# Performance work log

Measured on AMD Instinct MI355X. Metric: run time of the kernel, lower is better.

The kernel has to match this reference:

```python
import jax, jax.numpy as jnp
import numpy as np

NUM_SAMPLES = 32  # S: Gibbs chains per datapoint


def setup_inputs() -> dict:
    key = jax.random.key(0)
    ks = jax.random.split(key, 6)
    N, F, M, C = 2048, 1024, 128, 100
    x = jax.random.normal(ks[0], (N, F), dtype=jnp.float32)
    y = jax.random.randint(ks[1], (N,), 0, C)
    alpha_0 = jax.random.normal(ks[2], (M,), dtype=jnp.float32)
    alpha = jax.random.normal(ks[3], (M, F), dtype=jnp.float32) * jnp.float32(2.0 / np.sqrt(F))
    beta_0 = jax.random.normal(ks[4], (C,), dtype=jnp.float32)
    beta = jax.random.normal(ks[5], (C, M), dtype=jnp.float32) * jnp.float32(2.0 / np.sqrt(M))
    return {"x": x, "y": y, "alpha_0": alpha_0, "alpha": alpha, "beta_0": beta_0, "beta": beta}


def _gibbs_and_loglik(x, y, alpha_0, alpha, beta_0, beta):
    S = NUM_SAMPLES
    N = x.shape[0]
    C, M = beta.shape
    y_onehot = jax.nn.one_hot(y, C, dtype=x.dtype)           # (N, C)

    # compute_linear_pi / compute_pi_pos (pi_pos is no_grad in original)
    linear_pi = alpha_0[None, :] + x @ alpha.T               # (N, M)
    pi_pos = jax.lax.stop_gradient(jax.nn.sigmoid(linear_pi))

    key = jax.random.key(42)
    k_init, k_gibbs = jax.random.split(key)

    # init_sample2: Z ~ 2*Bernoulli(pi_pos) - 1, sampled S times  (no_grad)
    Z0 = 2.0 * jax.random.bernoulli(k_init, pi_pos, (S, N, M)).astype(x.dtype) - 1.0

    beta_sg = jax.lax.stop_gradient(beta)
    beta0_sg = jax.lax.stop_gradient(beta_0)

    # class logits for current Z; maintained incrementally across Gibbs steps
    lin0 = beta0_sg[None, None, :] + jnp.einsum('snm,cm->snc', Z0, beta_sg)  # (S, N, C)

    order = jnp.asarray(np.random.RandomState(0).permutation(M))  # fixed Gibbs sweep order
    keys = jax.random.split(k_gibbs, M)

    def step(carry, inp):
        Z, lin = carry
        j, k = inp
        zj = jnp.take(Z, j, axis=2)           # (S, N) current value of coord j
        bj = jnp.take(beta_sg, j, axis=1)     # (C,)
        pij = jnp.take(pi_pos, j, axis=1)     # (N,)
        # logits if coord j were +1 / -1 (rank-1 update of lin)
        lin_pos = lin + (1.0 - zj)[..., None] * bj
        lin_neg = lin + (-1.0 - zj)[..., None] * bj
        g_pos = jnp.exp(jnp.einsum('nc,snc->sn', y_onehot, lin_pos)) / jnp.sum(jnp.exp(lin_pos), axis=2)
        g_neg = jnp.exp(jnp.einsum('nc,snc->sn', y_onehot, lin_neg)) / jnp.sum(jnp.exp(lin_neg), axis=2)
        num = g_pos * pij[None, :]
        p = num / (num + g_neg * (1.0 - pij)[None, :])
        znew = 2.0 * jax.random.bernoulli(k, p).astype(lin.dtype) - 1.0  # (S, N)
        lin = lin + (znew - zj)[..., None] * bj
        Z = jax.lax.dynamic_update_index_in_dim(Z, znew, j, axis=2)
        return (Z, lin), None

    (Z, _), _ = jax.lax.scan(step, (Z0, lin0), (order, keys))
    Z = jax.lax.stop_gradient(Z)

    # moments
    EI = jnp.mean((Z + 1.0) * 0.5, axis=0)                   # (N, M)
    EII = jnp.mean(Z, axis=0)                                # (N, M)
    linear_gamma = beta_0[None, None, :] + jnp.einsum('snm,cm->snc', Z, beta)
    EIII = jnp.mean(jax.nn.logsumexp(linear_gamma, axis=2), axis=0)  # (N,)

    TermI = jnp.sum(y_onehot * (beta_0[None, :] + EII @ beta.T))
    TermII = jnp.sum(EIII)
    TermIII = jnp.sum(EI * linear_pi)
    TermIV = jnp.sum(jax.nn.softplus(linear_pi))             # log(1 + exp(linear_pi)), stable
    return TermI - TermII + TermIII - TermIV


def reference(x, y, alpha_0, alpha, beta_0, beta):
    return _gibbs_and_loglik(x, y, alpha_0, alpha, beta_0, beta)
```

## Files before the change

kernel.cpp:

```cpp
#include <hip/hip_runtime.h>
#include <hip/hip_fp16.h>
#include <stdint.h>

#define Nn 2048
#define Ff 1024
#define Mm 128
#define Cc 100
#define Ss 32
#define NM (Nn * Mm)
#define ELS 132
#define SCP 128
#define TOFF 16416
#define ESC 0.015625f
#define ESCLOG 4.15888308336f

typedef _Float16 h2f __attribute__((ext_vector_type(2)));
typedef short bf8 __attribute__((ext_vector_type(8)));
typedef float f32x4 __attribute__((ext_vector_type(4)));

__device__ __forceinline__ float qsum4(float x) {
  int a = __builtin_amdgcn_update_dpp(0, __builtin_bit_cast(int, x), 0xB1, 0xF, 0xF, false);
  float xf = x + __builtin_bit_cast(float, a);
  int b = __builtin_amdgcn_update_dpp(0, __builtin_bit_cast(int, xf), 0x4E, 0xF, 0xF, false);
  return xf + __builtin_bit_cast(float, b);
}

__device__ __forceinline__ float dot2f(h2f a, h2f b, float c) {
#if __has_builtin(__builtin_amdgcn_fdot2)
  return __builtin_amdgcn_fdot2(a, b, c, false);
#else
  return fmaf((float)a[0], (float)b[0], fmaf((float)a[1], (float)b[1], c));
#endif
}
__device__ __forceinline__ float d2(__half2 e, uint32_t v, float c) {
  return dot2f(__builtin_bit_cast(h2f, e), __builtin_bit_cast(h2f, v), c);
}
__device__ __forceinline__ __half2 m2(__half2 e, uint32_t v) {
  return __hmul2(e, __builtin_bit_cast(__half2, v));
}

__device__ __forceinline__ uint32_t hash32(uint32_t chain, uint32_t ctr) {
  uint32_t h = chain * 0x9E3779B9u ^ (ctr * 0x85EBCA6Bu);
  h ^= h >> 16; h *= 0x7FEB352Du;
  h ^= h >> 15; h *= 0x846CA68Bu;
  h ^= h >> 16;
  return h;
}
__device__ __forceinline__ float urand(uint32_t chain, uint32_t ctr) {
  return (float)(hash32(chain, ctr) >> 8) * (1.0f / 16777216.0f);
}
__device__ __forceinline__ uint32_t f2bf(float f) {
  uint32_t b = __builtin_bit_cast(uint32_t, f);
  return (b + 0x7FFFu + ((b >> 16) & 1u)) >> 16;
}
__device__ __forceinline__ float bf2f(uint16_t u) {
  uint32_t b = ((uint32_t)u) << 16;
  return __builtin_bit_cast(float, b);
}
__device__ __forceinline__ int cperm(int c) {
  return ((c >> 2) & 3) * 32 + (c >> 4) * 4 + (c & 3);
}
__device__ __forceinline__ int swz(int p) {
  int win = p >> 5, o = p & 31;
  return win * 32 + (((o >> 3) + win) & 3) * 8 + (o & 7);
}

__global__ __launch_bounds__(256) void k_lingemm(const float* __restrict__ x,
                                                 const float* __restrict__ alpha,
                                                 uint16_t* __restrict__ lpib) {
  __shared__ uint4 sA[256];
  __shared__ uint4 sB[1024];
  const int t = threadIdx.x;
  const int mt = blockIdx.x >> 2;
  const int ks = blockIdx.x & 3;
  const int m0 = mt * 32;
  const int w = t >> 6;
  const int l = t & 63;

  f32x4 acc[2][2] = {{{0.f, 0.f, 0.f, 0.f}, {0.f, 0.f, 0.f, 0.f}},
                     {{0.f, 0.f, 0.f, 0.f}, {0.f, 0.f, 0.f, 0.f}}};

  for (int kk = 0; kk < 4; ++kk) {
    const int k0 = ks * 256 + kk * 64;
    __syncthreads();
    {
      int row = t >> 3, c = t & 7;
      const float* px = &x[(m0 + row) * Ff + k0 + c * 8];
      float4 f0 = *(const float4*)px;
      float4 f1 = *(const float4*)(px + 4);
      uint4 v;
      v.x = f2bf(f0.x) | (f2bf(f0.y) << 16);
      v.y = f2bf(f0.z) | (f2bf(f0.w) << 16);
      v.z = f2bf(f1.x) | (f2bf(f1.y) << 16);
      v.w = f2bf(f1.z) | (f2bf(f1.w) << 16);
      sA[row * 8 + (c ^ (row & 7))] = v;
      #pragma unroll
      for (int rr = 0; rr < 4; ++rr) {
        int idx = t + rr * 256;
        int rowb = idx >> 3, cb = idx & 7;
        const float* pa = &alpha[rowb * Ff + k0 + cb * 8];
        float4 g0 = *(const float4*)pa;
        float4 g1 = *(const float4*)(pa + 4);
        uint4 vb;
        vb.x = f2bf(g0.x) | (f2bf(g0.y) << 16);
        vb.y = f2bf(g0.z) | (f2bf(g0.w) << 16);
        vb.z = f2bf(g1.x) | (f2bf(g1.y) << 16);
        vb.w = f2bf(g1.z) | (f2bf(g1.w) << 16);
        sB[rowb * 8 + (cb ^ (rowb & 7))] = vb;
      }
    }
    __syncthreads();
    #pragma unroll
    for (int kc = 0; kc < 2; ++kc) {
      int chunk = kc * 4 + (l >> 4);
      bf8 av[2], bv[2];
      #pragma unroll
      for (int fm = 0; fm < 2; ++fm) {
        int row = fm * 16 + (l & 15);
        av[fm] = __builtin_bit_cast(bf8, sA[row * 8 + (chunk ^ (row & 7))]);
      }
      #pragma unroll
      for (int fn = 0; fn < 2; ++fn) {
        int rowb = w * 32 + fn * 16 + (l & 15);
        bv[fn] = __builtin_bit_cast(bf8, sB[rowb * 8 + (chunk ^ (rowb & 7))]);
      }
      #pragma unroll
      for (int fm = 0; fm < 2; ++fm)
        #pragma unroll
        for (int fn = 0; fn < 2; ++fn)
          acc[fm][fn] = __builtin_amdgcn_mfma_f32_16x16x32_bf16(av[fm], bv[fn], acc[fm][fn], 0, 0, 0);
    }
  }
  #pragma unroll
  for (int fm = 0; fm < 2; ++fm)
    #pragma unroll
    for (int fn = 0; fn < 2; ++fn)
      #pragma unroll
      for (int r = 0; r < 4; ++r) {
        int row = m0 + fm * 16 + (l >> 4) * 4 + r;
        int col = w * 32 + fn * 16 + (l & 15);
        lpib[ks * NM + row * Mm + col] = (uint16_t)f2bf(acc[fm][fn][r]);
      }
}

#define PF(B0, B1, B2, B3, bit, j) {                                          \
    const __half* p_ = tab + ((bit) ? TOFF : 0) + (j) * SCP + hq * 32;        \
    B0 = *(const uint4*)(p_ + rot0);                                          \
    B1 = *(const uint4*)(p_ + rot1);                                          \
    B2 = *(const uint4*)(p_ + rot2);                                          \
    B3 = *(const uint2*)(p_ + rot3); }

#define STEP(B0, B1, B2, B3, zjp, eyel, u, bout) {                            \
    float d0_ = d2(E2_0, B0.x, 0.f), d1_ = d2(E2_1, B0.y, 0.f);               \
    float d2_ = d2(E2_2, B0.z, 0.f), d3_ = d2(E2_3, B0.w, 0.f);               \
    d0_ = d2(E2_4, B1.x, d0_); d1_ = d2(E2_5, B1.y, d1_);                     \
    d2_ = d2(E2_6, B1.z, d2_); d3_ = d2(E2_7, B1.w, d3_);                     \
    d0_ = d2(E2_8, B2.x, d0_); d1_ = d2(E2_9, B2.y, d1_);                     \
    d2_ = d2(E2_10, B2.z, d2_); d3_ = d2(E2_11, B2.w, d3_);                   \
    d0_ = d2(E2_12, B3.x, d0_); d1_ = d2(E2_13, B3.y, d1_);                   \
    float D_ = qsum4((d0_ + d1_) + (d2_ + d3_));                              \
    float Sp_ = (zjp) ? Sb : D_;                                              \
    float Sn_ = (zjp) ? D_ : Sb;                                              \
    float odds_ = (eyel) * Sn_ * __builtin_amdgcn_rcpf(Sp_);                  \
    uint32_t znp_ = ((u) * (1.0f + odds_) < odds_) ? 1u : 0u;                 \
    if ((znp_ ^ (zjp)) != 0u) {                                               \
      E2_0 = m2(E2_0, B0.x); E2_1 = m2(E2_1, B0.y);                           \
      E2_2 = m2(E2_2, B0.z); E2_3 = m2(E2_3, B0.w);                           \
      E2_4 = m2(E2_4, B1.x); E2_5 = m2(E2_5, B1.y);                           \
      E2_6 = m2(E2_6, B1.z); E2_7 = m2(E2_7, B1.w);                           \
      E2_8 = m2(E2_8, B2.x); E2_9 = m2(E2_9, B2.y);                           \
      E2_10 = m2(E2_10, B2.z); E2_11 = m2(E2_11, B2.w);                       \
      E2_12 = m2(E2_12, B3.x); E2_13 = m2(E2_13, B3.y);                       \
      Sb = D_;                                                                \
    }                                                                         \
    bout = znp_; }

#define MKE(k)                                                                \
  {                                                                           \
    float2 b0v = *(const float2*)&b0p[c0m + 2 * (k)];                         \
    float ea_ = __expf(acc[(2 * (k)) >> 2][(2 * (k)) & 3] + b0v.x) * ESC;     \
    float eb_ = __expf(acc[(2 * (k) + 1) >> 2][(2 * (k) + 1) & 3] + b0v.y) * ESC; \
    E2_##k = __floats2half2_rn(ea_, eb_);                                     \
  }

#define SHF(k) E2_##k = __builtin_bit_cast(__half2,                           \
    (uint32_t)__shfl((int)__builtin_bit_cast(uint32_t, E2_##k), src, 64));

__global__ __launch_bounds__(1024, 4) void k_gibbs(const float* __restrict__ beta0g,
                                                   const float* __restrict__ betag,
                                                   const int* __restrict__ yg,
                                                   const float* __restrict__ alpha0,
                                                   const uint16_t* __restrict__ lpib,
                                                   float* __restrict__ out) {
  __shared__ __attribute__((aligned(16))) char SM[79584];
  uint16_t* bsb = (uint16_t*)SM;
  __half* tab = (__half*)SM;
  float* elpi = (float*)(SM + 65600);
  float* lpil = (float*)(SM + 69824);
  uint32_t* zsl = (uint32_t*)(SM + 73920);
  float* lsel = (float*)(SM + 78016);
  int* yl = (int*)(SM + 79040);
  float* b0p = (float*)(SM + 79072);
  float* red = (float*)(SM + 65600);

  const int t = threadIdx.x;
  const int n0 = blockIdx.x * 8;
  const int L = t & 63;

  for (int idx = t; idx < 112 * 32; idx += 1024) {
    int row = idx >> 5, u = idx & 31;
    int rr = (row < Cc) ? row : 0;
    float4 v = *(const float4*)&betag[rr * Mm + u * 4];
    uint2 o;
    o.x = f2bf(v.x) | (f2bf(v.y) << 16);
    o.y = f2bf(v.z) | (f2bf(v.w) << 16);
    int k = u >> 1, sub = u & 1;
    int kp = k ^ (row & 15);
    *(uint2*)&bsb[row * 128 + kp * 8 + sub * 4] = o;
  }
  if (t < 128) b0p[cperm(t)] = (t < Cc) ? beta0g[t] : 0.0f;
  {
    int nls = t >> 7, j = t & 127;
    int g = (n0 + nls) * Mm + j;
    float lv = bf2f(lpib[g]) + bf2f(lpib[NM + g]) + bf2f(lpib[2 * NM + g]) +
               bf2f(lpib[3 * NM + g]) + alpha0[j];
    lpil[nls * Mm + j] = lv;
    elpi[nls * ELS + j] = __expf(lv);
  }
  if (t < 8) yl[t] = yg[n0 + t];
  __syncthreads();

  const int cl = t >> 2;
  const int hq = t & 3;
  const int nl = cl >> 5;
  const int s = cl & 31;
  const uint32_t chain = (uint32_t)((n0 + nl) * Ss + s);
  const int yv = yl[nl];

  uint32_t zz = 0;
  {
    #pragma unroll 1
    for (int b5 = 0; b5 < 32; ++b5) {
      int mloc = (b5 + hq * 8) & 31;
      int m = hq * 32 + mloc;
      float u = urand(chain, (uint32_t)m);
      float el = elpi[nl * ELS + m];
      zz |= (u * (1.0f + el) < el) ? (1u << mloc) : 0u;
    }
  }

  f32x4 acc[7];
  #pragma unroll
  for (int T = 0; T < 7; ++T) acc[T] = (f32x4){0.f, 0.f, 0.f, 0.f};
  {
    const int liw = L & 15, hw = L >> 4;
    #pragma unroll
    for (int ks = 0; ks < 4; ++ks) {
      uint32_t zw = (uint32_t)__shfl((int)zz, (liw << 2) | ks, 64);
      uint32_t bits8 = (zw >> (hw * 8)) & 0xFFu;
      uint4 pk;
      {
        uint32_t p0 = ((bits8 >> 0) & 1u) ? 0x3F80u : 0xBF80u;
        uint32_t p1 = ((bits8 >> 1) & 1u) ? 0x3F80u : 0xBF80u;
        uint32_t p2 = ((bits8 >> 2) & 1u) ? 0x3F80u : 0xBF80u;
        uint32_t p3 = ((bits8 >> 3) & 1u) ? 0x3F80u : 0xBF80u;
        uint32_t p4 = ((bits8 >> 4) & 1u) ? 0x3F80u : 0xBF80u;
        uint32_t p5 = ((bits8 >> 5) & 1u) ? 0x3F80u : 0xBF80u;
        uint32_t p6 = ((bits8 >> 6) & 1u) ? 0x3F80u : 0xBF80u;
        uint32_t p7 = ((bits8 >> 7) & 1u) ? 0x3F80u : 0xBF80u;
        pk.x = p0 | (p1 << 16); pk.y = p2 | (p3 << 16);
        pk.z = p4 | (p5 << 16); pk.w = p6 | (p7 << 16);
      }
      bf8 B = __builtin_bit_cast(bf8, pk);
      #pragma unroll
      for (int T = 0; T < 7; ++T) {
        int row = T * 16 + liw;
        int kk = ks * 4 + hw;
        bf8 A = __builtin_bit_cast(bf8, *(const uint4*)&bsb[row * 128 + (kk ^ (row & 15)) * 8]);
        acc[T] = __builtin_amdgcn_mfma_f32_16x16x32_bf16(A, B, acc[T], 0, 0, 0);
      }
    }
  }

  const __half2 HZERO = __builtin_bit_cast(__half2, 0u);
  __half2 E2_0, E2_1, E2_2, E2_3, E2_4, E2_5, E2_6, E2_7;
  __half2 E2_8, E2_9, E2_10, E2_11, E2_12, E2_13;
  {
    int c0m = (L >> 4) * 32;
    MKE(0) MKE(1) MKE(2) MKE(3) MKE(4) MKE(5) MKE(6)
    MKE(7) MKE(8) MKE(9) MKE(10) MKE(11) MKE(12) MKE(13)
    if ((L >> 4) != 0) { E2_12 = HZERO; E2_13 = HZERO; }
  }
  {
    int src = (L >> 2) | ((L & 3) << 4);
    SHF(0) SHF(1) SHF(2) SHF(3) SHF(4) SHF(5) SHF(6)
    SHF(7) SHF(8) SHF(9) SHF(10) SHF(11) SHF(12) SHF(13)
  }
  uint32_t zw0 = (uint32_t)__shfl((int)zz, (L & ~3) | 0, 64);
  uint32_t zw1 = (uint32_t)__shfl((int)zz, (L & ~3) | 1, 64);
  uint32_t zw2 = (uint32_t)__shfl((int)zz, (L & ~3) | 2, 64);
  uint32_t zw3 = (uint32_t)__shfl((int)zz, (L & ~3) | 3, 64);

  const uint32_t ONE2 = 0x3C003C00u;
  float Sb;
  {
    float d0_ = d2(E2_0, ONE2, 0.f), d1_ = d2(E2_1, ONE2, 0.f);
    float d2_ = d2(E2_2, ONE2, 0.f), d3_ = d2(E2_3, ONE2, 0.f);
    d0_ = d2(E2_4, ONE2, d0_); d1_ = d2(E2_5, ONE2, d1_);
    d2_ = d2(E2_6, ONE2, d2_); d3_ = d2(E2_7, ONE2, d3_);
    d0_ = d2(E2_8, ONE2, d0_); d1_ = d2(E2_9, ONE2, d1_);
    d2_ = d2(E2_10, ONE2, d2_); d3_ = d2(E2_11, ONE2, d3_);
    d0_ = d2(E2_12, ONE2, d0_); d1_ = d2(E2_13, ONE2, d1_);
    Sb = qsum4((d0_ + d1_) + (d2_ + d3_));
  }

  __syncthreads();
  for (int idx = t; idx < 32 * Cc; idx += 1024) {
    int j4 = idx / Cc;
    int c = idx - j4 * Cc;
    int ps = swz(cperm(c));
    float4 bv = *(const float4*)&betag[c * Mm + j4 * 4];
    int j = j4 * 4;
    tab[(j + 0) * SCP + ps] = __float2half(__expf(2.0f * bv.x));
    tab[TOFF + (j + 0) * SCP + ps] = __float2half(__expf(-2.0f * bv.x));
    tab[(j + 1) * SCP + ps] = __float2half(__expf(2.0f * bv.y));
    tab[TOFF + (j + 1) * SCP + ps] = __float2half(__expf(-2.0f * bv.y));
    tab[(j + 2) * SCP + ps] = __float2half(__expf(2.0f * bv.z));
    tab[TOFF + (j + 2) * SCP + ps] = __float2half(__expf(-2.0f * bv.z));
    tab[(j + 3) * SCP + ps] = __float2half(__expf(2.0f * bv.w));
    tab[TOFF + (j + 3) * SCP + ps] = __float2half(__expf(-2.0f * bv.w));
  }
  for (int idx = t; idx < Mm * 28; idx += 1024) {
    int j = idx / 28;
    int c = Cc + (idx - j * 28);
    int ps = swz(cperm(c));
    tab[j * SCP + ps] = __float2half(1.0f);
    tab[TOFF + j * SCP + ps] = __float2half(1.0f);
  }
  for (int idx = t; idx < Mm * 16; idx += 1024) {
    int j = idx >> 4;
    int win = (idx >> 2) & 3, o = 28 + (idx & 3);
    int ps = win * 32 + (((o >> 3) + win) & 3) * 8 + (o & 7);
    tab[j * SCP + ps] = __float2half(1.0f);
    tab[TOFF + j * SCP + ps] = __float2half(1.0f);
  }
  __syncthreads();

  const int pyv_s = swz(cperm(yv));
  const int rot0 = ((0 + hq) & 3) * 8;
  const int rot1 = ((1 + hq) & 3) * 8;
  const int rot2 = ((2 + hq) & 3) * 8;
  const int rot3 = ((3 + hq) & 3) * 8;

  uint4 va0, va1, va2, vb0, vb1, vb2;
  uint2 va3, vb3;

  PF(va0, va1, va2, va3, zw0 & 1u, 0)

  #pragma unroll 1
  for (int jb = 0; jb < Mm; jb += 4) {
    int w = jb >> 5;
    uint32_t zwv = (w == 0) ? zw0 : ((w == 1) ? zw1 : ((w == 2) ? zw2 : zw3));
    const int sh = jb & 31;
    uint32_t b0 = (zwv >> (sh + 0)) & 1u;
    uint32_t b1 = (zwv >> (sh + 1)) & 1u;
    uint32_t b2 = (zwv >> (sh + 2)) & 1u;
    uint32_t b3 = (zwv >> (sh + 3)) & 1u;
    uint32_t b4;
    if (sh == 28) {
      uint32_t nw = (w == 0) ? zw1 : ((w == 1) ? zw2 : ((w == 2) ? zw3 : 0u));
      b4 = nw & 1u;
    } else {
      b4 = (zwv >> (sh + 4)) & 1u;
    }
    float4 elv = *(const float4*)&elpi[nl * ELS + jb];
    float eyel0 = __half2float(tab[(jb + 0) * SCP + pyv_s]) * elv.x;
    float eyel1 = __half2float(tab[(jb + 1) * SCP + pyv_s]) * elv.y;
    float eyel2 = __half2float(tab[(jb + 2) * SCP + pyv_s]) * elv.z;
    float eyel3 = __half2float(tab[(jb + 3) * SCP + pyv_s]) * elv.w;
    uint32_t h1 = hash32(chain, 256u + (uint32_t)jb);
    uint32_t h2 = hash32(chain, 258u + (uint32_t)jb);
    float u0 = (float)(h1 & 0xFFFFu) * (1.0f / 65536.0f);
    float u1 = (float)(h1 >> 16) * (1.0f / 65536.0f);
    float u2 = (float)(h2 & 0xFFFFu) * (1.0f / 65536.0f);
    float u3 = (float)(h2 >> 16) * (1.0f / 65536.0f);

    PF(vb0, vb1, vb2, vb3, b1, jb + 1)
    STEP(va0, va1, va2, va3, b0, eyel0, u0, b0)
    PF(va0, va1, va2, va3, b2, jb + 2)
    STEP(vb0, vb1, vb2, vb3, b1, eyel1, u1, b1)
    PF(vb0, vb1, vb2, vb3, b3, jb + 3)
    STEP(va0, va1, va2, va3, b2, eyel2, u2, b2)
    PF(va0, va1, va2, va3, b4, (jb + 4) & 127)
    STEP(vb0, vb1, vb2, vb3, b3, eyel3, u3, b3)

    uint32_t nib = b0 | (b1 << 1) | (b2 << 2) | (b3 << 3);
    zwv = (zwv & ~(0xFu << sh)) | (nib << sh);
    if (w == 0) zw0 = zwv; else if (w == 1) zw1 = zwv;
    else if (w == 2) zw2 = zwv; else zw3 = zwv;
  }

  float Sf;
  {
    float d0_ = d2(E2_0, ONE2, 0.f), d1_ = d2(E2_1, ONE2, 0.f);
    float d2_ = d2(E2_2, ONE2, 0.f), d3_ = d2(E2_3, ONE2, 0.f);
    d0_ = d2(E2_4, ONE2, d0_); d1_ = d2(E2_5, ONE2, d1_);
    d2_ = d2(E2_6, ONE2, d2_); d3_ = d2(E2_7, ONE2, d3_);
    d0_ = d2(E2_8, ONE2, d0_); d1_ = d2(E2_9, ONE2, d1_);
    d2_ = d2(E2_10, ONE2, d2_); d3_ = d2(E2_11, ONE2, d3_);
    d0_ = d2(E2_12, ONE2, d0_); d1_ = d2(E2_13, ONE2, d1_);
    Sf = qsum4((d0_ + d1_) + (d2_ + d3_));
  }
  if (hq == 0) {
    lsel[cl] = __logf(Sf) + ESCLOG;
    zsl[cl * 4 + 0] = zw0; zsl[cl * 4 + 1] = zw1;
    zsl[cl * 4 + 2] = zw2; zsl[cl * 4 + 3] = zw3;
  }
  __syncthreads();

  {
    int nl2 = t >> 7;
    int mp = t & 127;
    int wsel = mp >> 5, sh0 = mp & 31;
    int cnt = 0;
    #pragma unroll 1
    for (int s2 = 0; s2 < 32; ++s2)
      cnt += (int)((zsl[(nl2 * 32 + s2) * 4 + wsel] >> sh0) & 1u);
    float EI = (float)cnt * (1.0f / 32.0f);
    float EII = 2.0f * EI - 1.0f;
    float l = lpil[nl2 * Mm + mp];
    int yv2 = yl[nl2];
    float bb = betag[yv2 * Mm + mp];
    float sp = (l > 20.0f) ? l : __logf(1.0f + __expf(l));
    float term = EII * bb + EI * l - sp;
    if (t < 256) term -= lsel[t] * (1.0f / 32.0f);
    if (t < 8) term += beta0g[yl[t]];
    red[t] = term;
  }
  __syncthreads();
  for (int off = 512; off > 0; off >>= 1) {
    if (t < off) red[t] += red[t + off];
    __syncthreads();
  }
  if (t == 0) atomicAdd(out, red[0]);
}

extern "C" void kernel_launch(void* const* d_in, const int* in_sizes, int n_in,
                              void* d_out, int out_size, void* d_ws, size_t ws_size,
                              hipStream_t stream) {
  const float* x = (const float*)d_in[0];
  const int* y = (const int*)d_in[1];
  const float* alpha0 = (const float*)d_in[2];
  const float* alpha = (const float*)d_in[3];
  const float* beta0 = (const float*)d_in[4];
  const float* beta = (const float*)d_in[5];
  float* out = (float*)d_out;

  uint16_t* lpib = (uint16_t*)d_ws;

  hipMemsetAsync(d_out, 0, sizeof(float), stream);
  k_lingemm<<<256, 256, 0, stream>>>(x, alpha, lpib);
  k_gibbs<<<256, 1024, 0, stream>>>(beta0, beta, y, alpha0, lpib, out);
}
```

Baseline: 96.81 us.

## Deepen Gibbs prefetch to four buffers and precompute per-coordinate y-factor LUT

Builds a per-datapoint shared-memory table holding exp(2*beta[y,j])*exp(lpi) once, replacing four fp16 table reads and multiplies per step group. The Gibbs sweep becomes an outer unrolled loop over the four z-words with an inner loop over groups of four coordinates. It keeps two pairs of prefetched table rows in flight instead of alternating one ahead, and uses sched_barriers to pin the order of loads and computation. The extra buffers raise register pressure and the kernel needs more LDS, which may limit occupancy at 1024-thread blocks.

```diff
diff --git a/kernel.cpp b/kernel.cpp
--- a/kernel.cpp
+++ b/kernel.cpp
@@ -192,7 +192,7 @@
                                                    const float* __restrict__ alpha0,
                                                    const uint16_t* __restrict__ lpib,
                                                    float* __restrict__ out) {
-  __shared__ __attribute__((aligned(16))) char SM[79584];
+  __shared__ __attribute__((aligned(16))) char SM[83808];
   uint16_t* bsb = (uint16_t*)SM;
   __half* tab = (__half*)SM;
   float* elpi = (float*)(SM + 65600);
@@ -201,6 +201,7 @@
   float* lsel = (float*)(SM + 78016);
   int* yl = (int*)(SM + 79040);
   float* b0p = (float*)(SM + 79072);
+  float* eyelLUT = (float*)(SM + 79584);
   float* red = (float*)(SM + 65600);
 
   const int t = threadIdx.x;
@@ -230,12 +231,17 @@
   if (t < 8) yl[t] = yg[n0 + t];
   __syncthreads();
 
+  {
+    int nl2 = t >> 7, j = t & 127;
+    float b = betag[yl[nl2] * Mm + j];
+    eyelLUT[nl2 * ELS + j] = __expf(2.0f * b) * elpi[nl2 * ELS + j];
+  }
+
   const int cl = t >> 2;
   const int hq = t & 3;
   const int nl = cl >> 5;
   const int s = cl & 31;
   const uint32_t chain = (uint32_t)((n0 + nl) * Ss + s);
-  const int yv = yl[nl];
 
   uint32_t zz = 0;
   {
@@ -346,56 +352,58 @@
   }
   __syncthreads();
 
-  const int pyv_s = swz(cperm(yv));
   const int rot0 = ((0 + hq) & 3) * 8;
   const int rot1 = ((1 + hq) & 3) * 8;
   const int rot2 = ((2 + hq) & 3) * 8;
   const int rot3 = ((3 + hq) & 3) * 8;
 
-  uint4 va0, va1, va2, vb0, vb1, vb2;
-  uint2 va3, vb3;
-
-  PF(va0, va1, va2, va3, zw0 & 1u, 0)
-
-  #pragma unroll 1
-  for (int jb = 0; jb < Mm; jb += 4) {
-    int w = jb >> 5;
+  uint4 sA00, sA01, sA02, sA10, sA11, sA12;
+  uint2 sA03, sA13;
+  uint4 sB00, sB01, sB02, sB10, sB11, sB12;
+  uint2 sB03, sB13;
+
+  PF(sA00, sA01, sA02, sA03, zw0 & 1u, 0)
+  PF(sA10, sA11, sA12, sA13, (zw0 >> 1) & 1u, 1)
+  float4 eycur = *(const float4*)&eyelLUT[nl * ELS];
+
+  #pragma unroll
+  for (int w = 0; w < 4; ++w) {
     uint32_t zwv = (w == 0) ? zw0 : ((w == 1) ? zw1 : ((w == 2) ? zw2 : zw3));
-    const int sh = jb & 31;
-    uint32_t b0 = (zwv >> (sh + 0)) & 1u;
-    uint32_t b1 = (zwv >> (sh + 1)) & 1u;
-    uint32_t b2 = (zwv >> (sh + 2)) & 1u;
-    uint32_t b3 = (zwv >> (sh + 3)) & 1u;
-    uint32_t b4;
-    if (sh == 28) {
-      uint32_t nw = (w == 0) ? zw1 : ((w == 1) ? zw2 : ((w == 2) ? zw3 : 0u));
-      b4 = nw & 1u;
-    } else {
-      b4 = (zwv >> (sh + 4)) & 1u;
+    const uint32_t nextw = (w == 0) ? zw1 : ((w == 1) ? zw2 : ((w == 2) ? zw3 : 0u));
+    #pragma unroll 1
+    for (int g = 0; g < 8; ++g) {
+      const int jb = w * 32 + g * 4;
+      const int sh = g * 4;
+      uint64_t win = (zwv >> sh) | ((uint64_t)nextw << (32 - sh));
+      uint32_t b0 = (uint32_t)win & 1u;
+      uint32_t b1 = ((uint32_t)(win >> 1)) & 1u;
+      uint32_t b2 = ((uint32_t)(win >> 2)) & 1u;
+      uint32_t b3 = ((uint32_t)(win >> 3)) & 1u;
+      uint32_t c4 = ((uint32_t)(win >> 4)) & 1u;
+      uint32_t c5 = ((uint32_t)(win >> 5)) & 1u;
+      uint32_t h1 = hash32(chain, 256u + (uint32_t)jb);
+      uint32_t h2 = hash32(chain, 258u + (uint32_t)jb);
+      float u0 = (float)(h1 & 0xFFFFu) * (1.0f / 65536.0f);
+      float u1 = (float)(h1 >> 16) * (1.0f / 65536.0f);
+      float u2 = (float)(h2 & 0xFFFFu) * (1.0f / 65536.0f);
+      float u3 = (float)(h2 >> 16) * (1.0f / 65536.0f);
+
+      PF(sB00, sB01, sB02, sB03, b2, jb + 2)
+      PF(sB10, sB11, sB12, sB13, b3, jb + 3)
+      __builtin_amdgcn_sched_barrier(0);
+      STEP(sA00, sA01, sA02, sA03, b0, eycur.x, u0, b0)
+      STEP(sA10, sA11, sA12, sA13, b1, eycur.y, u1, b1)
+      PF(sA00, sA01, sA02, sA03, c4, (jb + 4) & 127)
+      PF(sA10, sA11, sA12, sA13, c5, (jb + 5) & 127)
+      float4 eyn = *(const float4*)&eyelLUT[nl * ELS + ((jb + 4) & 127)];
+      __builtin_amdgcn_sched_barrier(0);
+      STEP(sB00, sB01, sB02, sB03, b2, eycur.z, u2, b2)
+      STEP(sB10, sB11, sB12, sB13, b3, eycur.w, u3, b3)
+      eycur = eyn;
+
+      uint32_t nib = b0 | (b1 << 1) | (b2 << 2) | (b3 << 3);
+      zwv = (zwv & ~(0xFu << sh)) | (nib << sh);
     }
-    float4 elv = *(const float4*)&elpi[nl * ELS + jb];
-    float eyel0 = __half2float(tab[(jb + 0) * SCP + pyv_s]) * elv.x;
-    float eyel1 = __half2float(tab[(jb + 1) * SCP + pyv_s]) * elv.y;
-    float eyel2 = __half2float(tab[(jb + 2) * SCP + pyv_s]) * elv.z;
-    float eyel3 = __half2float(tab[(jb + 3) * SCP + pyv_s]) * elv.w;
-    uint32_t h1 = hash32(chain, 256u + (uint32_t)jb);
-    uint32_t h2 = hash32(chain, 258u + (uint32_t)jb);
-    float u0 = (float)(h1 & 0xFFFFu) * (1.0f / 65536.0f);
-    float u1 = (float)(h1 >> 16) * (1.0f / 65536.0f);
-    float u2 = (float)(h2 & 0xFFFFu) * (1.0f / 65536.0f);
-    float u3 = (float)(h2 >> 16) * (1.0f / 65536.0f);
-
-    PF(vb0, vb1, vb2, vb3, b1, jb + 1)
-    STEP(va0, va1, va2, va3, b0, eyel0, u0, b0)
-    PF(va0, va1, va2, va3, b2, jb + 2)
-    STEP(vb0, vb1, vb2, vb3, b1, eyel1, u1, b1)
-    PF(vb0, vb1, vb2, vb3, b3, jb + 3)
-    STEP(va0, va1, va2, va3, b2, eyel2, u2, b2)
-    PF(va0, va1, va2, va3, b4, (jb + 4) & 127)
-    STEP(vb0, vb1, vb2, vb3, b3, eyel3, u3, b3)
-
-    uint32_t nib = b0 | (b1 << 1) | (b2 << 2) | (b3 << 3);
-    zwv = (zwv & ~(0xFu << sh)) | (nib << sh);
     if (w == 0) zw0 = zwv; else if (w == 1) zw1 = zwv;
     else if (w == 2) zw2 = zwv; else zw3 = zwv;
   }
```

After: 92.61 us. 4.3% less time.
